# Performance work log

Hardware: AMD Instinct MI355X
Metric: run time of the kernel (lower is better)

The kernel has to match this reference:

```python
import jax, jax.numpy as jnp
import numpy as np

N0, N1, N2 = 320000, 80000, 16000
E1, E2 = 800000, 160000
IN_C, HID, OUT_C = 128, 64, 48
H1, H2 = 4, 1
NEG_SLOPE = 0.2  # PyG GATv2Conv default leaky_relu slope


def _glorot(key, shape):
    fan_in = shape[0]
    return jax.random.normal(key, shape, jnp.float32) / jnp.sqrt(jnp.asarray(fan_in, jnp.float32))


def setup_inputs() -> dict:
    key = jax.random.key(0)
    ks = jax.random.split(key, 12)
    inp = {
        "x": jax.random.normal(ks[0], (N0, IN_C), jnp.float32),
        # layer 1: GATv2Conv(IN_C -> HID, heads=H1, concat=True)
        "Wl1": _glorot(ks[1], (IN_C, H1 * HID)),
        "bl1": jnp.zeros((H1 * HID,), jnp.float32),
        "Wr1": _glorot(ks[2], (IN_C, H1 * HID)),
        "br1": jnp.zeros((H1 * HID,), jnp.float32),
        "att1": jax.random.normal(ks[3], (H1, HID), jnp.float32) * 0.1,
        "bias1": jnp.zeros((H1 * HID,), jnp.float32),
        # layer 2: GATv2Conv(H1*HID -> OUT_C, heads=H2, concat=False)
        "Wl2": _glorot(ks[4], (H1 * HID, H2 * OUT_C)),
        "bl2": jnp.zeros((H2 * OUT_C,), jnp.float32),
        "Wr2": _glorot(ks[5], (H1 * HID, H2 * OUT_C)),
        "br2": jnp.zeros((H2 * OUT_C,), jnp.float32),
        "att2": jax.random.normal(ks[6], (H2, OUT_C), jnp.float32) * 0.1,
        "bias2": jnp.zeros((OUT_C,), jnp.float32),
        # sampled bipartite edge lists (edge j->i: src index into x_src, dst into x_dst)
        "src1": jax.random.randint(ks[7], (E1,), 0, N0, jnp.int32),
        "dst1": jax.random.randint(ks[8], (E1,), 0, N1, jnp.int32),
        "src2": jax.random.randint(ks[9], (E2,), 0, N1, jnp.int32),
        "dst2": jax.random.randint(ks[10], (E2,), 0, N2, jnp.int32),
        "n1": N1,
        "n2": N2,
    }
    return inp


def gatv2_conv(x_src, x_dst, src, dst, Wl, bl, Wr, br, att, bias, n_dst, concat):
    H, C = att.shape
    xl = (x_src @ Wl + bl).reshape(-1, H, C)   # [N_src, H, C] (source transform)
    xr = (x_dst @ Wr + br).reshape(-1, H, C)   # [N_dst, H, C] (target transform)
    e = xl[src] + xr[dst]                      # [E, H, C]
    e = jnp.where(e > 0, e, NEG_SLOPE * e)     # leaky_relu (GATv2: nonlinearity before att)
    alpha = jnp.einsum('ehc,hc->eh', e, att)   # [E, H] attention logits
    # softmax over edges sharing the same target node
    amax = jax.ops.segment_max(alpha, dst, num_segments=n_dst)
    ex = jnp.exp(alpha - amax[dst])
    denom = jax.ops.segment_sum(ex, dst, num_segments=n_dst)
    w = ex / (denom[dst] + 1e-16)              # [E, H]
    out = jax.ops.segment_sum(xl[src] * w[:, :, None], dst, num_segments=n_dst)  # [N_dst, H, C]
    out = out.reshape(n_dst, H * C) if concat else out.mean(axis=1)
    return out + bias


def reference(x, Wl1, bl1, Wr1, br1, att1, bias1, Wl2, bl2, Wr2, br2, att2, bias2,
              src1, dst1, src2, dst2, n1, n2):
    h = gatv2_conv(x, x[:n1], src1, dst1, Wl1, bl1, Wr1, br1, att1, bias1, n1, True)
    h = jax.nn.relu(h)
    # dropout is identity in eval mode
    h = gatv2_conv(h, h[:n2], src2, dst2, Wl2, bl2, Wr2, br2, att2, bias2, n2, False)
    return jax.nn.log_softmax(h, axis=-1)
```

## Files before the change

kernel.cpp:

```cpp
#include <hip/hip_runtime.h>
#include <hip/hip_bf16.h>

#define N0_  320000
#define N1_  80000
#define N2_  16000
#define INC_ 128
#define HID_ 64
#define H1_  4
#define C1_  256
#define OUT_ 48
#define NEG_ 0.2f

typedef __attribute__((ext_vector_type(8))) short bfrag8;
typedef __attribute__((ext_vector_type(4))) float ffrag4;

__device__ __forceinline__ float bf2f(unsigned short u){
  unsigned int v = ((unsigned int)u) << 16;
  return __uint_as_float(v);
}
__device__ __forceinline__ unsigned short f2bf(float f){
  unsigned int u = __float_as_uint(f);
  u += 0x7FFFu + ((u >> 16) & 1u);
  return (unsigned short)(u >> 16);
}

__global__ void transpose_to_bf16(const float* __restrict__ W,
                                  unsigned short* __restrict__ Wt, int K, int N){
  int idx = blockIdx.x*256 + threadIdx.x;
  if (idx >= K*N) return;
  int n = idx / K, k = idx - n*K;
  Wt[idx] = f2bf(W[(size_t)k*N + n]);
}

__global__ __launch_bounds__(256, 3) void gemm_mfma_k128n256(
    const float* __restrict__ X, const unsigned short* __restrict__ Wt,
    const float* __restrict__ bias, unsigned short* __restrict__ out)
{
  __shared__ unsigned short As[64][136];
  __shared__ unsigned short Cs[64][264];
  const int t = threadIdx.x;
  const int lane = t & 63, wave = t >> 6;
  const int row0 = blockIdx.x << 6;
  const int l15 = lane & 15, q = lane >> 4;
  const int wcol = wave << 6;

  bfrag8 bfr[4][4];
  #pragma unroll
  for (int nt = 0; nt < 4; ++nt)
    #pragma unroll
    for (int ks = 0; ks < 4; ++ks)
      bfr[nt][ks] = *(const bfrag8*)(Wt + (size_t)(wcol + (nt<<4) + l15)*128 + (ks<<5) + (q<<3));

  const int c4 = t & 31;
  #pragma unroll
  for (int i = 0; i < 8; ++i){
    int r = (i<<3) + (t>>5);
    float4 xv = *(const float4*)(X + ((size_t)(row0 + r) << 7) + (c4<<2));
    ushort4 s; s.x=f2bf(xv.x); s.y=f2bf(xv.y); s.z=f2bf(xv.z); s.w=f2bf(xv.w);
    *(ushort4*)(&As[r][c4<<2]) = s;
  }
  __syncthreads();

  ffrag4 z = {0.f, 0.f, 0.f, 0.f};
  ffrag4 acc[4][4];
  #pragma unroll
  for (int mt = 0; mt < 4; ++mt)
    #pragma unroll
    for (int nt = 0; nt < 4; ++nt) acc[mt][nt] = z;

  #pragma unroll
  for (int mt = 0; mt < 4; ++mt){
    #pragma unroll
    for (int ks = 0; ks < 4; ++ks){
      bfrag8 af = *(const bfrag8*)(&As[(mt<<4) + l15][(ks<<5) + (q<<3)]);
      #pragma unroll
      for (int nt = 0; nt < 4; ++nt)
        acc[mt][nt] = __builtin_amdgcn_mfma_f32_16x16x32_bf16(af, bfr[nt][ks], acc[mt][nt], 0, 0, 0);
    }
  }

  float bb[4];
  #pragma unroll
  for (int nt = 0; nt < 4; ++nt) bb[nt] = bias[wcol + (nt<<4) + l15];
  #pragma unroll
  for (int mt = 0; mt < 4; ++mt)
    #pragma unroll
    for (int nt = 0; nt < 4; ++nt)
      #pragma unroll
      for (int rg = 0; rg < 4; ++rg)
        Cs[(mt<<4) + (q<<2) + rg][wcol + (nt<<4) + l15] = f2bf(acc[mt][nt][rg] + bb[nt]);
  __syncthreads();
  #pragma unroll
  for (int i = 0; i < 8; ++i){
    int r = (i<<3) + (t>>5);
    *(bfrag8*)(out + ((size_t)(row0 + r) << 8) + (c4<<3)) = *(const bfrag8*)(&Cs[r][c4<<3]);
  }
}

__global__ __launch_bounds__(256) void gemm_mfma_k256n48(
    const unsigned short* __restrict__ Hin, const unsigned short* __restrict__ Wt,
    const float* __restrict__ bias, float* __restrict__ out)
{
  __shared__ unsigned short As2[64][264];
  __shared__ unsigned short Bs2[48][264];
  const int t = threadIdx.x;
  const int lane = t & 63, wave = t >> 6;
  const int row0 = blockIdx.x << 6;
  const int l15 = lane & 15, q = lane >> 4;

  const int c32 = t & 31;
  #pragma unroll
  for (int i = 0; i < 8; ++i){
    int r = (i<<3) + (t>>5);
    *(bfrag8*)(&As2[r][c32<<3]) = *(const bfrag8*)(Hin + ((size_t)(row0 + r) << 8) + (c32<<3));
  }
  #pragma unroll
  for (int i = 0; i < 6; ++i){
    int idx = i*256 + t;
    int r = idx >> 5, c = (idx & 31) << 3;
    *(bfrag8*)(&Bs2[r][c]) = *(const bfrag8*)(Wt + (size_t)r*256 + c);
  }
  __syncthreads();

  ffrag4 z = {0.f, 0.f, 0.f, 0.f};
  ffrag4 acc[3] = {z, z, z};
  #pragma unroll
  for (int ks = 0; ks < 8; ++ks){
    bfrag8 af = *(const bfrag8*)(&As2[(wave<<4) + l15][(ks<<5) + (q<<3)]);
    #pragma unroll
    for (int nt = 0; nt < 3; ++nt){
      bfrag8 bf = *(const bfrag8*)(&Bs2[(nt<<4) + l15][(ks<<5) + (q<<3)]);
      acc[nt] = __builtin_amdgcn_mfma_f32_16x16x32_bf16(af, bf, acc[nt], 0, 0, 0);
    }
  }
  #pragma unroll
  for (int nt = 0; nt < 3; ++nt){
    int col = (nt<<4) + l15;
    float bb = bias[col];
    #pragma unroll
    for (int rg = 0; rg < 4; ++rg){
      int row = row0 + (wave<<4) + (q<<2) + rg;
      out[(size_t)row*OUT_ + col] = acc[nt][rg] + bb;
    }
  }
}

__global__ void hist_k(const int* __restrict__ dst, int* __restrict__ counts, int E){
  int i = blockIdx.x*blockDim.x + threadIdx.x;
  if (i < E) atomicAdd(&counts[dst[i]], 1);
}

__global__ __launch_bounds__(256) void scan_local(const int* __restrict__ in,
    int* __restrict__ excl, int* __restrict__ partials, int n){
  __shared__ int s[256];
  int t = threadIdx.x, i = blockIdx.x*256 + t;
  int v = (i < n) ? in[i] : 0;
  s[t] = v; __syncthreads();
  #pragma unroll
  for (int off = 1; off < 256; off <<= 1){
    int u = (t >= off) ? s[t-off] : 0;
    __syncthreads();
    s[t] += u; __syncthreads();
  }
  if (i < n) excl[i] = s[t] - v;
  if (t == 255) partials[blockIdx.x] = s[255];
}

__global__ __launch_bounds__(512) void scan_partials(int* __restrict__ partials, int nb){
  __shared__ int s[512];
  int t = threadIdx.x;
  int v = (t < nb) ? partials[t] : 0;
  s[t] = v; __syncthreads();
  #pragma unroll
  for (int off = 1; off < 512; off <<= 1){
    int u = (t >= off) ? s[t-off] : 0;
    __syncthreads();
    s[t] += u; __syncthreads();
  }
  if (t < nb) partials[t] = s[t] - v;
}

__global__ void scan_finalize(int* __restrict__ excl, const int* __restrict__ partials,
    int* __restrict__ cursor, int n){
  int i = blockIdx.x*256 + threadIdx.x;
  if (i >= n) return;
  int o = excl[i] + partials[blockIdx.x];
  excl[i] = o; cursor[i] = o;
}

__global__ void scatter_k(const int* __restrict__ src, const int* __restrict__ dst,
    int* __restrict__ cursor, int* __restrict__ perm, int E){
  int i = blockIdx.x*blockDim.x + threadIdx.x;
  if (i >= E) return;
  int pos = atomicAdd(&cursor[dst[i]], 1);
  perm[pos] = src[i];
}

__global__ __launch_bounds__(256) void gat_aggregate1(
    const unsigned short* __restrict__ xl, const unsigned short* __restrict__ xr,
    const int* __restrict__ offsets, const int* __restrict__ counts,
    const int* __restrict__ perm, const float* __restrict__ att,
    const float* __restrict__ bias, unsigned short* __restrict__ hout, int n)
{
  int node = (blockIdx.x << 2) + (threadIdx.x >> 6);
  if (node >= n) return;
  int lane = threadIdx.x & 63;
  int off = ((lane >> 4) << 6) + ((lane & 15) << 2);
  ushort4 rv = *(const ushort4*)(xr + (size_t)node*C1_ + off);
  float r0 = bf2f(rv.x), r1 = bf2f(rv.y), r2 = bf2f(rv.z), r3 = bf2f(rv.w);
  float4 av = *(const float4*)(att + off);
  float a0 = 0.f, a1 = 0.f, a2 = 0.f, a3 = 0.f, den = 0.f;
  int st = offsets[node], cnt = counts[node];
  for (int j = 0; j < cnt; ++j){
    int s = perm[st + j];
    ushort4 xv = *(const ushort4*)(xl + (size_t)s*C1_ + off);
    float x0 = bf2f(xv.x), x1 = bf2f(xv.y), x2 = bf2f(xv.z), x3 = bf2f(xv.w);
    float e0 = x0 + r0; e0 = e0 > 0.f ? e0 : NEG_*e0;
    float e1 = x1 + r1; e1 = e1 > 0.f ? e1 : NEG_*e1;
    float e2 = x2 + r2; e2 = e2 > 0.f ? e2 : NEG_*e2;
    float e3 = x3 + r3; e3 = e3 > 0.f ? e3 : NEG_*e3;
    float p = e0*av.x + e1*av.y + e2*av.z + e3*av.w;
    p += __shfl_xor(p, 1);
    p += __shfl_xor(p, 2);
    p += __shfl_xor(p, 4);
    p += __shfl_xor(p, 8);
    float ex = expf(p);
    den += ex;
    a0 = fmaf(ex, x0, a0); a1 = fmaf(ex, x1, a1);
    a2 = fmaf(ex, x2, a2); a3 = fmaf(ex, x3, a3);
  }
  float w = 1.f / (den + 1e-16f);
  float4 b4 = *(const float4*)(bias + off);
  ushort4 o;
  o.x = f2bf(fmaxf(fmaf(a0, w, b4.x), 0.f));
  o.y = f2bf(fmaxf(fmaf(a1, w, b4.y), 0.f));
  o.z = f2bf(fmaxf(fmaf(a2, w, b4.z), 0.f));
  o.w = f2bf(fmaxf(fmaf(a3, w, b4.w), 0.f));
  *(ushort4*)(hout + (size_t)node*C1_ + off) = o;
}

__global__ __launch_bounds__(256) void gat_aggregate2(
    const float* __restrict__ xl, const float* __restrict__ xr,
    const int* __restrict__ offsets, const int* __restrict__ counts,
    const int* __restrict__ perm, const float* __restrict__ att,
    const float* __restrict__ bias, float* __restrict__ out, int n)
{
  int node = (blockIdx.x << 2) + (threadIdx.x >> 6);
  if (node >= n) return;
  int lane = threadIdx.x & 63;
  bool act = lane < OUT_;
  float r = act ? xr[(size_t)node*OUT_ + lane] : 0.f;
  float a = act ? att[lane] : 0.f;
  float acc = 0.f, den = 0.f;
  int st = offsets[node], cnt = counts[node];
  for (int j = 0; j < cnt; ++j){
    int s = perm[st + j];
    float xv = act ? xl[(size_t)s*OUT_ + lane] : 0.f;
    float e = xv + r; e = e > 0.f ? e : NEG_*e;
    float p = e * a;
    #pragma unroll
    for (int o = 1; o < 64; o <<= 1) p += __shfl_xor(p, o);
    float ex = expf(p);
    den += ex;
    acc = fmaf(ex, xv, acc);
  }
  float v = acc / (den + 1e-16f) + (act ? bias[lane] : 0.f);
  float m = act ? v : -3.0e38f;
  #pragma unroll
  for (int o = 1; o < 64; o <<= 1) m = fmaxf(m, __shfl_xor(m, o));
  float ex = act ? expf(v - m) : 0.f;
  float ss = ex;
  #pragma unroll
  for (int o = 1; o < 64; o <<= 1) ss += __shfl_xor(ss, o);
  float ls = logf(ss);
  if (act) out[(size_t)node*OUT_ + lane] = v - m - ls;
}

extern "C" void kernel_launch(void* const* d_in, const int* in_sizes, int n_in,
                              void* d_out, int out_size, void* d_ws, size_t ws_size,
                              hipStream_t stream)
{
  const float* x    = (const float*)d_in[0];
  const float* Wl1  = (const float*)d_in[1];
  const float* bl1  = (const float*)d_in[2];
  const float* Wr1  = (const float*)d_in[3];
  const float* br1  = (const float*)d_in[4];
  const float* att1 = (const float*)d_in[5];
  const float* bias1= (const float*)d_in[6];
  const float* Wl2  = (const float*)d_in[7];
  const float* bl2  = (const float*)d_in[8];
  const float* Wr2  = (const float*)d_in[9];
  const float* br2  = (const float*)d_in[10];
  const float* att2 = (const float*)d_in[11];
  const float* bias2= (const float*)d_in[12];
  const int* src1 = (const int*)d_in[13];
  const int* dst1 = (const int*)d_in[14];
  const int* src2 = (const int*)d_in[15];
  const int* dst2 = (const int*)d_in[16];
  const int E1 = in_sizes[13];
  const int E2 = in_sizes[15];
  (void)n_in; (void)out_size; (void)ws_size;

  char* ws = (char*)d_ws;
  unsigned short* xl1  = (unsigned short*)(ws + 0LL);
  unsigned short* xr1  = (unsigned short*)(ws + 163840000LL);
  unsigned short* hbuf = (unsigned short*)(ws + 204800000LL);
  float* xl2    = (float*)(ws + 245760000LL);
  float* xr2    = (float*)(ws + 261120000LL);
  int*   perm1  = (int*)  (ws + 264192000LL);
  int*   perm2  = (int*)  (ws + 267392000LL);
  int*   cnt1   = (int*)  (ws + 268032000LL);
  int*   cnt2   = (int*)  (ws + 268352000LL);
  int*   off1   = (int*)  (ws + 268416000LL);
  int*   cur1   = (int*)  (ws + 268736000LL);
  int*   off2   = (int*)  (ws + 269056000LL);
  int*   cur2   = (int*)  (ws + 269120000LL);
  int*   part1  = (int*)  (ws + 269184000LL);
  int*   part2  = (int*)  (ws + 269186048LL);
  unsigned short* Wt1l = (unsigned short*)(ws + 269188096LL);
  unsigned short* Wt1r = (unsigned short*)(ws + 269253632LL);
  unsigned short* Wt2l = (unsigned short*)(ws + 269319168LL);
  unsigned short* Wt2r = (unsigned short*)(ws + 269343744LL);

  hipMemsetAsync(ws + 268032000LL, 0, 384000LL, stream);

  const int nb1 = (N1_ + 255) / 256;
  const int nb2 = (N2_ + 255) / 256;

  transpose_to_bf16<<<128, 256, 0, stream>>>(Wl1, Wt1l, INC_, C1_);
  transpose_to_bf16<<<128, 256, 0, stream>>>(Wr1, Wt1r, INC_, C1_);
  transpose_to_bf16<<< 48, 256, 0, stream>>>(Wl2, Wt2l, C1_, OUT_);
  transpose_to_bf16<<< 48, 256, 0, stream>>>(Wr2, Wt2r, C1_, OUT_);

  gemm_mfma_k128n256<<<N0_/64, 256, 0, stream>>>(x, Wt1l, bl1, xl1);
  gemm_mfma_k128n256<<<N1_/64, 256, 0, stream>>>(x, Wt1r, br1, xr1);
  hist_k       <<<(E1+255)/256, 256, 0, stream>>>(dst1, cnt1, E1);
  scan_local   <<<nb1, 256, 0, stream>>>(cnt1, off1, part1, N1_);
  scan_partials<<<1, 512, 0, stream>>>(part1, nb1);
  scan_finalize<<<nb1, 256, 0, stream>>>(off1, part1, cur1, N1_);
  scatter_k    <<<(E1+255)/256, 256, 0, stream>>>(src1, dst1, cur1, perm1, E1);
  gat_aggregate1<<<(N1_+3)/4, 256, 0, stream>>>(xl1, xr1, off1, cnt1, perm1,
                                                att1, bias1, hbuf, N1_);
  gemm_mfma_k256n48<<<N1_/64, 256, 0, stream>>>(hbuf, Wt2l, bl2, xl2);
  gemm_mfma_k256n48<<<N2_/64, 256, 0, stream>>>(hbuf, Wt2r, br2, xr2);
  hist_k       <<<(E2+255)/256, 256, 0, stream>>>(dst2, cnt2, E2);
  scan_local   <<<nb2, 256, 0, stream>>>(cnt2, off2, part2, N2_);
  scan_partials<<<1, 512, 0, stream>>>(part2, nb2);
  scan_finalize<<<nb2, 256, 0, stream>>>(off2, part2, cur2, N2_);
  scatter_k    <<<(E2+255)/256, 256, 0, stream>>>(src2, dst2, cur2, perm2, E2);
  gat_aggregate2<<<(N2_+3)/4, 256, 0, stream>>>(xl2, xr2, off2, cnt2, perm2,
                                                att2, bias2, (float*)d_out, N2_);
}
```

Baseline: 631.7 us.

## Process multiple edges per wave in GAT aggregation with wider vector loads

Both aggregation kernels now split each wave into slots that handle different edges at once: two edges per wave with 16-byte bf16 loads in layer 1, and four edges per wave in layer 2. Neighbor indices are loaded 64 at a time and broadcast with shuffles, and partial sums are combined across slots at the end. The layer-2 GEMM output is padded to 64 columns with zeroed tail columns so rows can be read as aligned float4. The aim is more memory-level parallelism per wave and fewer serialized perm loads, at the cost of extra cross-slot reductions, a larger workspace, and lower-precision __expf/__logf.

```diff
diff --git a/kernel.cpp b/kernel.cpp
--- a/kernel.cpp
+++ b/kernel.cpp
@@ -9,6 +9,7 @@
 #define H1_  4
 #define C1_  256
 #define OUT_ 48
+#define OUTP_ 64
 #define NEG_ 0.2f
 
 typedef __attribute__((ext_vector_type(8))) short bfrag8;
@@ -22,6 +23,10 @@
   unsigned int u = __float_as_uint(f);
   u += 0x7FFFu + ((u >> 16) & 1u);
   return (unsigned short)(u >> 16);
+}
+__device__ __forceinline__ void unpack2(unsigned int u, float& lo, float& hi){
+  lo = __uint_as_float(u << 16);
+  hi = __uint_as_float(u & 0xffff0000u);
 }
 
 __global__ void transpose_to_bf16(const float* __restrict__ W,
@@ -140,8 +145,13 @@
     #pragma unroll
     for (int rg = 0; rg < 4; ++rg){
       int row = row0 + (wave<<4) + (q<<2) + rg;
-      out[(size_t)row*OUT_ + col] = acc[nt][rg] + bb;
-    }
+      out[(size_t)row*OUTP_ + col] = acc[nt][rg] + bb;
+    }
+  }
+  #pragma unroll
+  for (int rg = 0; rg < 4; ++rg){
+    int row = row0 + (wave<<4) + (q<<2) + rg;
+    out[(size_t)row*OUTP_ + 48 + l15] = 0.f;
   }
 }
 
@@ -204,39 +214,71 @@
 {
   int node = (blockIdx.x << 2) + (threadIdx.x >> 6);
   if (node >= n) return;
-  int lane = threadIdx.x & 63;
-  int off = ((lane >> 4) << 6) + ((lane & 15) << 2);
-  ushort4 rv = *(const ushort4*)(xr + (size_t)node*C1_ + off);
-  float r0 = bf2f(rv.x), r1 = bf2f(rv.y), r2 = bf2f(rv.z), r3 = bf2f(rv.w);
-  float4 av = *(const float4*)(att + off);
-  float a0 = 0.f, a1 = 0.f, a2 = 0.f, a3 = 0.f, den = 0.f;
-  int st = offsets[node], cnt = counts[node];
-  for (int j = 0; j < cnt; ++j){
-    int s = perm[st + j];
-    ushort4 xv = *(const ushort4*)(xl + (size_t)s*C1_ + off);
-    float x0 = bf2f(xv.x), x1 = bf2f(xv.y), x2 = bf2f(xv.z), x3 = bf2f(xv.w);
-    float e0 = x0 + r0; e0 = e0 > 0.f ? e0 : NEG_*e0;
-    float e1 = x1 + r1; e1 = e1 > 0.f ? e1 : NEG_*e1;
-    float e2 = x2 + r2; e2 = e2 > 0.f ? e2 : NEG_*e2;
-    float e3 = x3 + r3; e3 = e3 > 0.f ? e3 : NEG_*e3;
-    float p = e0*av.x + e1*av.y + e2*av.z + e3*av.w;
-    p += __shfl_xor(p, 1);
-    p += __shfl_xor(p, 2);
-    p += __shfl_xor(p, 4);
-    p += __shfl_xor(p, 8);
-    float ex = expf(p);
-    den += ex;
-    a0 = fmaf(ex, x0, a0); a1 = fmaf(ex, x1, a1);
-    a2 = fmaf(ex, x2, a2); a3 = fmaf(ex, x3, a3);
-  }
-  float w = 1.f / (den + 1e-16f);
-  float4 b4 = *(const float4*)(bias + off);
-  ushort4 o;
-  o.x = f2bf(fmaxf(fmaf(a0, w, b4.x), 0.f));
-  o.y = f2bf(fmaxf(fmaf(a1, w, b4.y), 0.f));
-  o.z = f2bf(fmaxf(fmaf(a2, w, b4.z), 0.f));
-  o.w = f2bf(fmaxf(fmaf(a3, w, b4.w), 0.f));
-  *(ushort4*)(hout + (size_t)node*C1_ + off) = o;
+  const int lane = threadIdx.x & 63;
+  const int slot = lane >> 5;
+  const int sub  = lane & 31;
+  const int elem = sub << 3;
+  const unsigned int ebyte = (unsigned)elem << 1;
+  const char* xlb = (const char*)xl;
+
+  uint4 ru = *(const uint4*)(xr + ((size_t)node << 8) + elem);
+  float r[8];
+  unpack2(ru.x, r[0], r[1]); unpack2(ru.y, r[2], r[3]);
+  unpack2(ru.z, r[4], r[5]); unpack2(ru.w, r[6], r[7]);
+  float4 al = *(const float4*)(att + elem);
+  float4 ah = *(const float4*)(att + elem + 4);
+  float a[8] = {al.x, al.y, al.z, al.w, ah.x, ah.y, ah.z, ah.w};
+
+  float acc[8] = {0,0,0,0,0,0,0,0};
+  float den = 0.f;
+  const int st = offsets[node], cnt = counts[node];
+
+  for (int jb = 0; jb < cnt; jb += 64){
+    int m = cnt - jb; if (m > 64) m = 64;
+    int pv = (lane < m) ? perm[st + jb + lane] : 0;
+    #pragma unroll 2
+    for (int j = 0; j < m; j += 2){
+      int idx = j + slot;
+      int s = __shfl(pv, idx);
+      uint4 xu = *(const uint4*)(xlb + (((unsigned)s << 9) + ebyte));
+      float x[8];
+      unpack2(xu.x, x[0], x[1]); unpack2(xu.y, x[2], x[3]);
+      unpack2(xu.z, x[4], x[5]); unpack2(xu.w, x[6], x[7]);
+      float p = 0.f;
+      #pragma unroll
+      for (int i = 0; i < 8; ++i){
+        float v = x[i] + r[i];
+        float e = fmaf(NEG_, fminf(v, 0.f), fmaxf(v, 0.f));
+        p = fmaf(e, a[i], p);
+      }
+      p += __shfl_xor(p, 1);
+      p += __shfl_xor(p, 2);
+      p += __shfl_xor(p, 4);
+      float ex = __expf(p);
+      ex = (idx < m) ? ex : 0.f;
+      den += ex;
+      #pragma unroll
+      for (int i = 0; i < 8; ++i) acc[i] = fmaf(ex, x[i], acc[i]);
+    }
+  }
+  den += __shfl_xor(den, 32);
+  #pragma unroll
+  for (int i = 0; i < 8; ++i) acc[i] += __shfl_xor(acc[i], 32);
+
+  if (slot == 0){
+    float w = 1.f / (den + 1e-16f);
+    float4 bl = *(const float4*)(bias + elem);
+    float4 bh = *(const float4*)(bias + elem + 4);
+    float b[8] = {bl.x, bl.y, bl.z, bl.w, bh.x, bh.y, bh.z, bh.w};
+    unsigned int o[4];
+    #pragma unroll
+    for (int i = 0; i < 4; ++i){
+      unsigned short lo = f2bf(fmaxf(fmaf(acc[2*i],   w, b[2*i]),   0.f));
+      unsigned short hi = f2bf(fmaxf(fmaf(acc[2*i+1], w, b[2*i+1]), 0.f));
+      o[i] = (unsigned)lo | ((unsigned)hi << 16);
+    }
+    *(uint4*)(hout + ((size_t)node << 8) + elem) = make_uint4(o[0], o[1], o[2], o[3]);
+  }
 }
 
 __global__ __launch_bounds__(256) void gat_aggregate2(
@@ -247,33 +289,64 @@
 {
   int node = (blockIdx.x << 2) + (threadIdx.x >> 6);
   if (node >= n) return;
-  int lane = threadIdx.x & 63;
-  bool act = lane < OUT_;
-  float r = act ? xr[(size_t)node*OUT_ + lane] : 0.f;
-  float a = act ? att[lane] : 0.f;
-  float acc = 0.f, den = 0.f;
-  int st = offsets[node], cnt = counts[node];
-  for (int j = 0; j < cnt; ++j){
-    int s = perm[st + j];
-    float xv = act ? xl[(size_t)s*OUT_ + lane] : 0.f;
-    float e = xv + r; e = e > 0.f ? e : NEG_*e;
-    float p = e * a;
-    #pragma unroll
-    for (int o = 1; o < 64; o <<= 1) p += __shfl_xor(p, o);
-    float ex = expf(p);
-    den += ex;
-    acc = fmaf(ex, xv, acc);
-  }
-  float v = acc / (den + 1e-16f) + (act ? bias[lane] : 0.f);
-  float m = act ? v : -3.0e38f;
-  #pragma unroll
-  for (int o = 1; o < 64; o <<= 1) m = fmaxf(m, __shfl_xor(m, o));
-  float ex = act ? expf(v - m) : 0.f;
-  float ss = ex;
-  #pragma unroll
-  for (int o = 1; o < 64; o <<= 1) ss += __shfl_xor(ss, o);
-  float ls = logf(ss);
-  if (act) out[(size_t)node*OUT_ + lane] = v - m - ls;
+  const int lane = threadIdx.x & 63;
+  const int slot = lane >> 4;
+  const int sub  = lane & 15;
+  const bool realc = sub < 12;
+
+  float4 r = *(const float4*)(xr + (size_t)node*OUTP_ + (sub<<2));
+  float4 a = realc ? *(const float4*)(att + (sub<<2)) : make_float4(0,0,0,0);
+  float4 acc = make_float4(0,0,0,0);
+  float den = 0.f;
+  const int st = offsets[node], cnt = counts[node];
+
+  for (int jb = 0; jb < cnt; jb += 64){
+    int m = cnt - jb; if (m > 64) m = 64;
+    int pv = (lane < m) ? perm[st + jb + lane] : 0;
+    #pragma unroll 2
+    for (int j = 0; j < m; j += 4){
+      int idx = j + slot;
+      int s = __shfl(pv, idx);
+      float4 xv = *(const float4*)(xl + (size_t)((unsigned)s*OUTP_ + (sub<<2)));
+      float v0 = xv.x + r.x, v1 = xv.y + r.y, v2 = xv.z + r.z, v3 = xv.w + r.w;
+      float p;
+      p = fmaf(a.x, fmaf(NEG_, fminf(v0,0.f), fmaxf(v0,0.f)), 0.f);
+      p = fmaf(a.y, fmaf(NEG_, fminf(v1,0.f), fmaxf(v1,0.f)), p);
+      p = fmaf(a.z, fmaf(NEG_, fminf(v2,0.f), fmaxf(v2,0.f)), p);
+      p = fmaf(a.w, fmaf(NEG_, fminf(v3,0.f), fmaxf(v3,0.f)), p);
+      p += __shfl_xor(p, 1);
+      p += __shfl_xor(p, 2);
+      p += __shfl_xor(p, 4);
+      p += __shfl_xor(p, 8);
+      float ex = __expf(p);
+      ex = (idx < m) ? ex : 0.f;
+      den += ex;
+      acc.x = fmaf(ex, xv.x, acc.x); acc.y = fmaf(ex, xv.y, acc.y);
+      acc.z = fmaf(ex, xv.z, acc.z); acc.w = fmaf(ex, xv.w, acc.w);
+    }
+  }
+  den += __shfl_xor(den, 16); den += __shfl_xor(den, 32);
+  acc.x += __shfl_xor(acc.x, 16); acc.x += __shfl_xor(acc.x, 32);
+  acc.y += __shfl_xor(acc.y, 16); acc.y += __shfl_xor(acc.y, 32);
+  acc.z += __shfl_xor(acc.z, 16); acc.z += __shfl_xor(acc.z, 32);
+  acc.w += __shfl_xor(acc.w, 16); acc.w += __shfl_xor(acc.w, 32);
+
+  float w = 1.f / (den + 1e-16f);
+  float4 b = realc ? *(const float4*)(bias + (sub<<2)) : make_float4(0,0,0,0);
+  float v0 = fmaf(acc.x, w, b.x), v1 = fmaf(acc.y, w, b.y);
+  float v2 = fmaf(acc.z, w, b.z), v3 = fmaf(acc.w, w, b.w);
+
+  float mx = realc ? fmaxf(fmaxf(v0, v1), fmaxf(v2, v3)) : -3.0e38f;
+  mx = fmaxf(mx, __shfl_xor(mx, 1)); mx = fmaxf(mx, __shfl_xor(mx, 2));
+  mx = fmaxf(mx, __shfl_xor(mx, 4)); mx = fmaxf(mx, __shfl_xor(mx, 8));
+  float es = realc ? (__expf(v0-mx) + __expf(v1-mx) + __expf(v2-mx) + __expf(v3-mx)) : 0.f;
+  es += __shfl_xor(es, 1); es += __shfl_xor(es, 2);
+  es += __shfl_xor(es, 4); es += __shfl_xor(es, 8);
+  float ls = __logf(es);
+  if (slot == 0 && realc){
+    float4 o = make_float4(v0-mx-ls, v1-mx-ls, v2-mx-ls, v3-mx-ls);
+    *(float4*)(out + (size_t)node*OUT_ + (sub<<2)) = o;
+  }
 }
 
 extern "C" void kernel_launch(void* const* d_in, const int* in_sizes, int n_in,
@@ -305,24 +378,24 @@
   unsigned short* xl1  = (unsigned short*)(ws + 0LL);
   unsigned short* xr1  = (unsigned short*)(ws + 163840000LL);
   unsigned short* hbuf = (unsigned short*)(ws + 204800000LL);
-  float* xl2    = (float*)(ws + 245760000LL);
-  float* xr2    = (float*)(ws + 261120000LL);
-  int*   perm1  = (int*)  (ws + 264192000LL);
-  int*   perm2  = (int*)  (ws + 267392000LL);
-  int*   cnt1   = (int*)  (ws + 268032000LL);
-  int*   cnt2   = (int*)  (ws + 268352000LL);
-  int*   off1   = (int*)  (ws + 268416000LL);
-  int*   cur1   = (int*)  (ws + 268736000LL);
-  int*   off2   = (int*)  (ws + 269056000LL);
-  int*   cur2   = (int*)  (ws + 269120000LL);
-  int*   part1  = (int*)  (ws + 269184000LL);
-  int*   part2  = (int*)  (ws + 269186048LL);
-  unsigned short* Wt1l = (unsigned short*)(ws + 269188096LL);
-  unsigned short* Wt1r = (unsigned short*)(ws + 269253632LL);
-  unsigned short* Wt2l = (unsigned short*)(ws + 269319168LL);
-  unsigned short* Wt2r = (unsigned short*)(ws + 269343744LL);
-
-  hipMemsetAsync(ws + 268032000LL, 0, 384000LL, stream);
+  float* xl2p   = (float*)(ws + 245760000LL);
+  float* xr2p   = (float*)(ws + 266240000LL);
+  int*   perm1  = (int*)  (ws + 270336000LL);
+  int*   perm2  = (int*)  (ws + 273536000LL);
+  int*   cnt1   = (int*)  (ws + 274176000LL);
+  int*   cnt2   = (int*)  (ws + 274496000LL);
+  int*   off1   = (int*)  (ws + 274560000LL);
+  int*   cur1   = (int*)  (ws + 274880000LL);
+  int*   off2   = (int*)  (ws + 275200000LL);
+  int*   cur2   = (int*)  (ws + 275264000LL);
+  int*   part1  = (int*)  (ws + 275328000LL);
+  int*   part2  = (int*)  (ws + 275330048LL);
+  unsigned short* Wt1l = (unsigned short*)(ws + 275332096LL);
+  unsigned short* Wt1r = (unsigned short*)(ws + 275397632LL);
+  unsigned short* Wt2l = (unsigned short*)(ws + 275463168LL);
+  unsigned short* Wt2r = (unsigned short*)(ws + 275487744LL);
+
+  hipMemsetAsync(ws + 274176000LL, 0, 384000LL, stream);
 
   const int nb1 = (N1_ + 255) / 256;
   const int nb2 = (N2_ + 255) / 256;
@@ -334,20 +407,25 @@
 
   gemm_mfma_k128n256<<<N0_/64, 256, 0, stream>>>(x, Wt1l, bl1, xl1);
   gemm_mfma_k128n256<<<N1_/64, 256, 0, stream>>>(x, Wt1r, br1, xr1);
+
   hist_k       <<<(E1+255)/256, 256, 0, stream>>>(dst1, cnt1, E1);
   scan_local   <<<nb1, 256, 0, stream>>>(cnt1, off1, part1, N1_);
   scan_partials<<<1, 512, 0, stream>>>(part1, nb1);
   scan_finalize<<<nb1, 256, 0, stream>>>(off1, part1, cur1, N1_);
   scatter_k    <<<(E1+255)/256, 256, 0, stream>>>(src1, dst1, cur1, perm1, E1);
+
   gat_aggregate1<<<(N1_+3)/4, 256, 0, stream>>>(xl1, xr1, off1, cnt1, perm1,
                                                 att1, bias1, hbuf, N1_);
-  gemm_mfma_k256n48<<<N1_/64, 256, 0, stream>>>(hbuf, Wt2l, bl2, xl2);
-  gemm_mfma_k256n48<<<N2_/64, 256, 0, stream>>>(hbuf, Wt2r, br2, xr2);
+
+  gemm_mfma_k256n48<<<N1_/64, 256, 0, stream>>>(hbuf, Wt2l, bl2, xl2p);
+  gemm_mfma_k256n48<<<N2_/64, 256, 0, stream>>>(hbuf, Wt2r, br2, xr2p);
+
   hist_k       <<<(E2+255)/256, 256, 0, stream>>>(dst2, cnt2, E2);
   scan_local   <<<nb2, 256, 0, stream>>>(cnt2, off2, part2, N2_);
   scan_partials<<<1, 512, 0, stream>>>(part2, nb2);
   scan_finalize<<<nb2, 256, 0, stream>>>(off2, part2, cur2, N2_);
   scatter_k    <<<(E2+255)/256, 256, 0, stream>>>(src2, dst2, cur2, perm2, E2);
-  gat_aggregate2<<<(N2_+3)/4, 256, 0, stream>>>(xl2, xr2, off2, cnt2, perm2,
+
+  gat_aggregate2<<<(N2_+3)/4, 256, 0, stream>>>(xl2p, xr2p, off2, cnt2, perm2,
                                                 att2, bias2, (float*)d_out, N2_);
 }
```

New measurement: 552.3 us. 1.14x faster.
